# Optimization experiments

Measured on AMD Instinct MI355X. Metric: run time of the kernel, lower is better.

Reference implementation:

```python
import jax, jax.numpy as jnp
import numpy as np

NU, NI = 16384, 8192          # num_users, num_items
DK, DM = 64, 64               # embed_k, embed_k_multimod
DV, DT = 4096, 384            # visual / textual feature dims
TOP_K = 10
N_LAYERS = 1                  # item-graph propagation layers
N_UI_LAYERS = 2               # user-item LGConv layers
L_M = 0.7
E = 524288                    # user-item interactions (doubled to symmetric edges)


def build_sim(x):
    # cosine similarity: row-normalize then x @ x.T  -> [N, N]
    xn = x / jnp.linalg.norm(x, axis=-1, keepdims=True)
    return xn @ xn.T


def build_knn(sim, k):
    # keep top-k values per row, zero elsewhere (torch topk + scatter_)
    vals, idx = jax.lax.top_k(sim, k)
    rows = jnp.arange(sim.shape[0])[:, None]
    return jnp.zeros_like(sim).at[rows, idx].set(vals)


def normalized_laplacian(adj):
    # D^{-1/2} A D^{-1/2}; inf (zero-degree) -> 0, applied as row/col scaling
    d = adj.sum(-1)
    dis = jnp.where(d > 0, jax.lax.rsqrt(jnp.where(d > 0, d, 1.0)), 0.0)
    return adj * dis[:, None] * dis[None, :]


def l2_normalize(x, axis=-1, eps=1e-12):
    n = jnp.linalg.norm(x, axis=axis, keepdims=True)
    return x / jnp.maximum(n, eps)


def setup_inputs() -> dict:
    key = jax.random.key(0)
    ks = jax.random.split(key, 8)
    Gu = jax.random.normal(ks[0], (NU, DK), jnp.float32) * 0.1
    Gi = jax.random.normal(ks[1], (NI, DK), jnp.float32) * 0.1
    feat_v = jax.random.normal(ks[2], (NI, DV), jnp.float32)
    feat_t = jax.random.normal(ks[3], (NI, DT), jnp.float32)
    W_v = jax.random.normal(ks[4], (DV, DM), jnp.float32) / np.sqrt(DV)
    b_v = jnp.zeros((DM,), jnp.float32)
    W_t = jax.random.normal(ks[5], (DT, DM), jnp.float32) / np.sqrt(DT)
    b_t = jnp.zeros((DM,), jnp.float32)
    importance_weights = jnp.full((2,), 0.5, jnp.float32)
    # precomputed per-modality normalized laplacians from raw (detached) features
    Sim_v = normalized_laplacian(build_knn(build_sim(feat_v), TOP_K))
    Sim_t = normalized_laplacian(build_knn(build_sim(feat_t), TOP_K))
    # symmetric bipartite user-item edge list (items offset by NU)
    u = jax.random.randint(ks[6], (E,), 0, NU)
    i = jax.random.randint(ks[7], (E,), 0, NI) + NU
    edge_index = jnp.stack([jnp.concatenate([u, i]), jnp.concatenate([i, u])])
    return dict(Gu=Gu, Gi=Gi, feat_v=feat_v, feat_t=feat_t, W_v=W_v, b_v=b_v,
                W_t=W_t, b_t=b_t, importance_weights=importance_weights,
                Sim_v=Sim_v, Sim_t=Sim_t, edge_index=edge_index)


def propagate(Gu, Gi, feat_v, feat_t, W_v, b_v, W_t, b_t,
              importance_weights, Sim_v, Sim_t, edge_index):
    w = jax.nn.softmax(importance_weights)
    learned = jnp.zeros((NI, NI), jnp.float32)
    original = jnp.zeros((NI, NI), jnp.float32)
    for m, (feat, W, b, Sim) in enumerate(
            [(feat_v, W_v, b_v, Sim_v), (feat_t, W_t, b_t, Sim_t)]):
        proj = feat @ W + b                                  # [NI, DM]
        learned = learned + w[m] * build_knn(build_sim(proj), TOP_K)
        original = original + w[m] * Sim
    Si = (1.0 - L_M) * normalized_laplacian(learned) + L_M * original
    # item-graph propagation
    item_emb = Gi
    for _ in range(N_LAYERS):
        item_emb = Si @ item_emb                              # [NI, DK]
    # user-item LGConv (normalize=False => plain sum aggregation)
    src, dst = edge_index[0], edge_index[1]
    all_emb = [jnp.concatenate([Gu, Gi], 0)]                  # [NU+NI, DK]
    for _ in range(N_UI_LAYERS):
        agg = jax.ops.segment_sum(all_emb[-1][src], dst, num_segments=NU + NI)
        all_emb.append(l2_normalize(agg, axis=1))
    mean_emb = jnp.stack(all_emb, 1).mean(1)
    gu, gi = mean_emb[:NU], mean_emb[NU:]
    return gu, gi + l2_normalize(item_emb, axis=1)


def reference(Gu, Gi, feat_v, feat_t, W_v, b_v, W_t, b_t,
              importance_weights, Sim_v, Sim_t, edge_index):
    return propagate(Gu, Gi, feat_v, feat_t, W_v, b_v, W_t, b_t,
                     importance_weights, Sim_v, Sim_t, edge_index)
```

## Files before the change

### kernel.cpp

```cpp
#include <hip/hip_runtime.h>
#include <hip/hip_bf16.h>

#define NU 16384
#define NI 8192
#define TOPK 10
#define NTOT (NU + NI)
#define OCAP 64
#define NSEG 4
#define CSEG (NI / NSEG)
#define NGRP 512
#define MAXSEL 16

typedef short short8v __attribute__((ext_vector_type(8)));
typedef float float4v __attribute__((ext_vector_type(4)));

__device__ __forceinline__ float warp64_sum(float v) {
#pragma unroll
  for (int m = 32; m >= 1; m >>= 1) v += __shfl_xor(v, m);
  return v;
}

__device__ __forceinline__ unsigned int umap(float f) {
  unsigned int b = __float_as_uint(f);
  return b ^ ((b & 0x80000000u) ? 0xFFFFFFFFu : 0x80000000u);
}

__global__ __launch_bounds__(256) void proj_partial_kernel(
    const float* __restrict__ feat, const float* __restrict__ W,
    float* __restrict__ partial, int D, int kchunk) {
  __shared__ float sA[64][32];
  __shared__ float sB[64][68];
  const int tid = threadIdx.x;
  const int r0 = blockIdx.x * 32;
  const int ks = blockIdx.y;
  const int kb0v = ks * kchunk;
  const int rg = tid >> 4, cg = tid & 15;
  const int rA = tid & 31, kbA = (tid >> 5) * 8;
  const int kB = tid & 63, cbB = (tid >> 6) * 16;
  float acc[2][4] = {{0, 0, 0, 0}, {0, 0, 0, 0}};
  for (int kc = kb0v; kc < kb0v + kchunk; kc += 64) {
    const float* fp = feat + (size_t)(r0 + rA) * D + kc + kbA;
    float4 p0 = *(const float4*)fp;
    float4 p1 = *(const float4*)(fp + 4);
    sA[kbA + 0][rA] = p0.x; sA[kbA + 1][rA] = p0.y;
    sA[kbA + 2][rA] = p0.z; sA[kbA + 3][rA] = p0.w;
    sA[kbA + 4][rA] = p1.x; sA[kbA + 5][rA] = p1.y;
    sA[kbA + 6][rA] = p1.z; sA[kbA + 7][rA] = p1.w;
    const float* wp = W + (size_t)(kc + kB) * 64 + cbB;
    float4 q0 = *(const float4*)(wp + 0);
    float4 q1 = *(const float4*)(wp + 4);
    float4 q2 = *(const float4*)(wp + 8);
    float4 q3 = *(const float4*)(wp + 12);
    *(float4*)&sB[kB][cbB + 0] = q0;
    *(float4*)&sB[kB][cbB + 4] = q1;
    *(float4*)&sB[kB][cbB + 8] = q2;
    *(float4*)&sB[kB][cbB + 12] = q3;
    __syncthreads();
#pragma unroll 8
    for (int k = 0; k < 64; ++k) {
      float2 a = *(const float2*)&sA[k][rg * 2];
      float4 bv = *(const float4*)&sB[k][cg * 4];
      acc[0][0] += a.x * bv.x; acc[0][1] += a.x * bv.y;
      acc[0][2] += a.x * bv.z; acc[0][3] += a.x * bv.w;
      acc[1][0] += a.y * bv.x; acc[1][1] += a.y * bv.y;
      acc[1][2] += a.y * bv.z; acc[1][3] += a.y * bv.w;
    }
    __syncthreads();
  }
#pragma unroll
  for (int rr = 0; rr < 2; ++rr) {
    float4 o = make_float4(acc[rr][0], acc[rr][1], acc[rr][2], acc[rr][3]);
    *(float4*)(partial + ((size_t)ks * NI + r0 + rg * 2 + rr) * 64 + cg * 4) = o;
  }
}

__global__ __launch_bounds__(256) void proj_reduce_kernel(
    const float* __restrict__ partial, const float* __restrict__ b, int ksplit,
    float* __restrict__ xn, ushort* __restrict__ hi, ushort* __restrict__ lo) {
  const int row = blockIdx.x * 4 + (threadIdx.x >> 6);
  const int col = threadIdx.x & 63;
  float acc = b[col];
  for (int ks = 0; ks < ksplit; ++ks)
    acc += partial[((size_t)ks * NI + row) * 64 + col];
  float ss = warp64_sum(acc * acc);
  float v = acc * (1.0f / sqrtf(ss));
  xn[(size_t)row * 64 + col] = v;
  __hip_bfloat16 hb = __float2bfloat16(v);
  float hf = __bfloat162float(hb);
  __hip_bfloat16 lb = __float2bfloat16(v - hf);
  hi[(size_t)row * 64 + col] = *(ushort*)&hb;
  lo[(size_t)row * 64 + col] = *(ushort*)&lb;
}

__global__ __launch_bounds__(256) void sim_tilemax_kernel(
    const ushort* __restrict__ hiV, const ushort* __restrict__ loV,
    const ushort* __restrict__ hiT, const ushort* __restrict__ loT,
    float* __restrict__ tmax) {
  const int m = blockIdx.z;
  const ushort* hi = m ? hiT : hiV;
  const ushort* lo = m ? loT : loV;
  const int seg = blockIdx.y;
  const int c_base = seg * CSEG;
  const int r_base = blockIdx.x * 64;
  __shared__ ushort sH[64][64];
  __shared__ ushort sL[64][64];
  const int tid = threadIdx.x;
  const int wave = tid >> 6, lane = tid & 63;
  const int lr = lane & 15, lg = lane >> 4;
  const int my_row = r_base + wave * 16 + lr;
  short8v bh[2], bl[2];
  {
    const ushort* rp = hi + (size_t)my_row * 64 + lg * 8;
    bh[0] = *(const short8v*)(rp);
    bh[1] = *(const short8v*)(rp + 32);
    const ushort* rp2 = lo + (size_t)my_row * 64 + lg * 8;
    bl[0] = *(const short8v*)(rp2);
    bl[1] = *(const short8v*)(rp2 + 32);
  }
  float* tbase = tmax + ((size_t)m * NI + my_row) * NGRP + seg * (CSEG / 16);

  const int sc = tid >> 2, sq = (tid & 3) * 32;
  const int sw = (sc & 7) << 4;
  for (int c0 = 0; c0 < CSEG; c0 += 64) {
    __syncthreads();
    const char* gh = (const char*)(hi + (size_t)(c_base + c0 + sc) * 64);
    const char* gl2 = (const char*)(lo + (size_t)(c_base + c0 + sc) * 64);
    *(float4*)((char*)&sH[sc][0] + (sq ^ sw)) = *(const float4*)(gh + sq);
    *(float4*)((char*)&sH[sc][0] + ((sq + 16) ^ sw)) = *(const float4*)(gh + sq + 16);
    *(float4*)((char*)&sL[sc][0] + (sq ^ sw)) = *(const float4*)(gl2 + sq);
    *(float4*)((char*)&sL[sc][0] + ((sq + 16) ^ sw)) = *(const float4*)(gl2 + sq + 16);
    __syncthreads();
#pragma unroll
    for (int s = 0; s < 4; ++s) {
      const int ca = s * 16 + lr;
      const int cw = (ca & 7) << 4;
      const int kb0 = (lg * 16) ^ cw;
      const int kb1 = (lg * 16 + 64) ^ cw;
      short8v ah0 = *(const short8v*)((const char*)&sH[ca][0] + kb0);
      short8v ah1 = *(const short8v*)((const char*)&sH[ca][0] + kb1);
      short8v al0 = *(const short8v*)((const char*)&sL[ca][0] + kb0);
      short8v al1 = *(const short8v*)((const char*)&sL[ca][0] + kb1);
      float4v acc = {0.f, 0.f, 0.f, 0.f};
      acc = __builtin_amdgcn_mfma_f32_16x16x32_bf16(ah0, bh[0], acc, 0, 0, 0);
      acc = __builtin_amdgcn_mfma_f32_16x16x32_bf16(ah1, bh[1], acc, 0, 0, 0);
      acc = __builtin_amdgcn_mfma_f32_16x16x32_bf16(ah0, bl[0], acc, 0, 0, 0);
      acc = __builtin_amdgcn_mfma_f32_16x16x32_bf16(ah1, bl[1], acc, 0, 0, 0);
      acc = __builtin_amdgcn_mfma_f32_16x16x32_bf16(al0, bh[0], acc, 0, 0, 0);
      acc = __builtin_amdgcn_mfma_f32_16x16x32_bf16(al1, bh[1], acc, 0, 0, 0);
      float gm = fmaxf(fmaxf(acc[0], acc[1]), fmaxf(acc[2], acc[3]));
      gm = fmaxf(gm, __shfl_xor(gm, 16));
      gm = fmaxf(gm, __shfl_xor(gm, 32));
      if (lg == 0) tbase[(c0 >> 4) + s] = gm;
    }
  }
}

__global__ __launch_bounds__(256) void tile_rescore_kernel(
    const float* __restrict__ xn_v, const float* __restrict__ xn_t,
    const float* __restrict__ tmax,
    float* __restrict__ tkvV, int* __restrict__ tkiV,
    float* __restrict__ tkvT, int* __restrict__ tkiT) {
  const int bid = blockIdx.x;
  const int m = bid >> 13;
  const int row = bid & (NI - 1);
  const float* xn = m ? xn_t : xn_v;
  const int tid = threadIdx.x;
  __shared__ int ssel[MAXSEL];
  __shared__ float4 srq[16];
  __shared__ float sval[MAXSEL * 16];
  __shared__ int scol[MAXSEL * 16];
  __shared__ float lv[32];
  __shared__ int lc[32];
  __shared__ int lnum;
  if (tid < 64) {
    const int lane = tid;
    const float4* tmr4 = (const float4*)(tmax + ((size_t)m * NI + row) * NGRP);
    float4 t0 = tmr4[lane];
    float4 t1 = tmr4[64 + lane];
    unsigned int uv[8] = {umap(t0.x), umap(t0.y), umap(t0.z), umap(t0.w),
                          umap(t1.x), umap(t1.y), umap(t1.z), umap(t1.w)};
    unsigned long long blo = 0, bhi = 0x100000000ull;
    unsigned int taub = 0;
    for (int it = 0; it < 34; ++it) {
      unsigned int mid = (unsigned int)((blo + bhi) >> 1);
      int cnt = 0;
#pragma unroll
      for (int j = 0; j < 8; ++j) cnt += __popcll(__ballot(uv[j] >= mid));
      if (cnt >= 12) {
        taub = mid;
        if (cnt <= MAXSEL) break;
        blo = (unsigned long long)mid + 1;
      } else {
        bhi = mid;
      }
      if (blo >= bhi) break;
    }
    unsigned long long bj[8];
    int base[8];
    int tot = 0;
#pragma unroll
    for (int j = 0; j < 8; ++j) {
      bj[j] = __ballot(uv[j] >= taub);
      base[j] = tot;
      tot += __popcll(bj[j]);
    }
    if (lane < MAXSEL) ssel[lane] = -1;
    unsigned long long ltm = (1ull << lane) - 1ull;
#pragma unroll
    for (int j = 0; j < 8; ++j) {
      if (uv[j] >= taub) {
        int pos = base[j] + __popcll(bj[j] & ltm);
        if (pos < MAXSEL) {
          int g = (j < 4) ? (lane * 4 + j) : (256 + lane * 4 + (j - 4));
          ssel[pos] = g;
        }
      }
    }
  } else if (tid < 80) {
    srq[tid - 64] = ((const float4*)(xn + (size_t)row * 64))[tid - 64];
  }
  __syncthreads();
  {
    const int gsel = ssel[tid >> 4];
    const bool valid = (gsel >= 0);
    const int c = valid ? (gsel * 16 + (tid & 15)) : 0;
    const float4* cp = (const float4*)(xn + (size_t)c * 64);
    float acc = 0.0f;
#pragma unroll
    for (int k = 0; k < 16; ++k) {
      float4 a = srq[k];
      float4 bv = cp[k];
      acc += a.x * bv.x; acc += a.y * bv.y; acc += a.z * bv.z; acc += a.w * bv.w;
    }
    sval[tid] = valid ? acc : -3.0e38f;
    scol[tid] = valid ? c : 0x7fffffff;
  }
  __syncthreads();
  if (tid < 64) {
    const int lane = tid;
    float fv[4];
    int fc[4];
    unsigned int uv4[4];
#pragma unroll
    for (int k = 0; k < 4; ++k) {
      fv[k] = sval[lane + 64 * k];
      fc[k] = scol[lane + 64 * k];
      uv4[k] = umap(fv[k]);
    }
    unsigned long long blo = 0, bhi = 0x100000000ull;
    unsigned int taub = 0;
    for (int it = 0; it < 34; ++it) {
      unsigned int mid = (unsigned int)((blo + bhi) >> 1);
      int cnt = 0;
#pragma unroll
      for (int k = 0; k < 4; ++k) cnt += __popcll(__ballot(uv4[k] >= mid));
      if (cnt >= TOPK) {
        taub = mid;
        if (cnt == TOPK) break;
        blo = (unsigned long long)mid + 1;
      } else {
        bhi = mid;
      }
      if (blo >= bhi) break;
    }
    unsigned long long bk[4];
    int base[4];
    int tot = 0;
#pragma unroll
    for (int k = 0; k < 4; ++k) {
      bk[k] = __ballot(uv4[k] >= taub);
      base[k] = tot;
      tot += __popcll(bk[k]);
    }
    float* tv = m ? tkvT : tkvV;
    int* ti = m ? tkiT : tkiV;
    unsigned long long ltm = (1ull << lane) - 1ull;
    if (tot == TOPK) {
#pragma unroll
      for (int k = 0; k < 4; ++k) {
        if (uv4[k] >= taub) {
          int pos = base[k] + __popcll(bk[k] & ltm);
          tv[(size_t)row * TOPK + pos] = fv[k];
          ti[(size_t)row * TOPK + pos] = fc[k];
        }
      }
    } else {
#pragma unroll
      for (int k = 0; k < 4; ++k) {
        if (uv4[k] >= taub) {
          int pos = base[k] + __popcll(bk[k] & ltm);
          if (pos < 32) { lv[pos] = fv[k]; lc[pos] = fc[k]; }
        }
      }
      if (lane == 0) lnum = (tot < 32) ? tot : 32;
      if (lane == 0) {
        int n = lnum;
        unsigned int used = 0;
        for (int q = 0; q < TOPK; ++q) {
          float bv = -3.0e38f;
          int bc = 0x7fffffff, bi = -1;
          for (int i2 = 0; i2 < n; ++i2) {
            if (used & (1u << i2)) continue;
            if (lv[i2] > bv || (lv[i2] == bv && lc[i2] < bc)) {
              bv = lv[i2]; bc = lc[i2]; bi = i2;
            }
          }
          used |= (1u << bi);
          tv[(size_t)row * TOPK + q] = bv;
          ti[(size_t)row * TOPK + q] = bc;
        }
      }
    }
  }
}

__global__ void dis_kernel(const float* __restrict__ tkv_v, const float* __restrict__ tkv_t,
                           const float* __restrict__ iw, float* __restrict__ dis) {
  int r = blockIdx.x * blockDim.x + threadIdx.x;
  if (r >= NI) return;
  float ea = expf(iw[0]), eb = expf(iw[1]);
  float w0 = ea / (ea + eb), w1 = eb / (ea + eb);
  float s0 = 0.f, s1 = 0.f;
  for (int j = 0; j < TOPK; ++j) { s0 += tkv_v[r * TOPK + j]; s1 += tkv_t[r * TOPK + j]; }
  float d = w0 * s0 + w1 * s1;
  dis[r] = (d > 0.0f) ? (1.0f / sqrtf(d)) : 0.0f;
}

__global__ __launch_bounds__(256) void scan_sim_kernel(
    const float* __restrict__ Sv, const float* __restrict__ St,
    const float* __restrict__ iw, int* __restrict__ ocols,
    float* __restrict__ ow, int* __restrict__ ocnt) {
  const int lane = threadIdx.x & 63;
  const int row = blockIdx.x * 4 + (threadIdx.x >> 6);
  float ea = expf(iw[0]), eb = expf(iw[1]);
  float wA = 0.7f * ea / (ea + eb), wB = 0.7f * eb / (ea + eb);
  int cnt = 0;
  int* oc = ocols + (size_t)row * OCAP;
  float* op = ow + (size_t)row * OCAP;
#pragma unroll 1
  for (int m = 0; m < 2; ++m) {
    const float* S = m ? St : Sv;
    float wgt = m ? wB : wA;
    const float4* rp = (const float4*)(S + (size_t)row * NI);
    for (int it = 0; it < NI / 256; ++it) {
      float4 v = rp[it * 64 + lane];
      int cb = it * 256 + lane * 4;
#pragma unroll
      for (int j = 0; j < 4; ++j) {
        float x = (j == 0) ? v.x : (j == 1) ? v.y : (j == 2) ? v.z : v.w;
        bool nz = (x != 0.0f);
        unsigned long long mk = __ballot(nz);
        int pre = __popcll(mk & ((1ull << lane) - 1ull));
        if (nz) {
          int p = cnt + pre;
          if (p < OCAP) { oc[p] = cb + j; op[p] = wgt * x; }
        }
        cnt += __popcll(mk);
      }
    }
  }
  if (lane == 0) ocnt[row] = (cnt < OCAP) ? cnt : OCAP;
}

__global__ __launch_bounds__(256) void item_emb_kernel(
    const float* __restrict__ Gi,
    const float* __restrict__ tkv_v, const int* __restrict__ tki_v,
    const float* __restrict__ tkv_t, const int* __restrict__ tki_t,
    const float* __restrict__ dis, const int* __restrict__ ocols,
    const float* __restrict__ ow, const int* __restrict__ ocnt,
    const float* __restrict__ iw, float* __restrict__ nitem) {
  const int d = threadIdx.x & 63;
  const int row = blockIdx.x * 4 + (threadIdx.x >> 6);
  float ea = expf(iw[0]), eb = expf(iw[1]);
  float w0 = ea / (ea + eb), w1 = eb / (ea + eb);
  float disr = dis[row];
  float acc = 0.0f;
#pragma unroll 1
  for (int m = 0; m < 2; ++m) {
    const float* tv = m ? tkv_t : tkv_v;
    const int* ti = m ? tki_t : tki_v;
    float wm = (m ? w1 : w0) * 0.3f * disr;
    for (int j = 0; j < TOPK; ++j) {
      float val = tv[(size_t)row * TOPK + j];
      int c = ti[(size_t)row * TOPK + j];
      acc += wm * val * dis[c] * Gi[(size_t)c * 64 + d];
    }
  }
  int cn = ocnt[row];
  for (int j = 0; j < cn; ++j) {
    int c = ocols[(size_t)row * OCAP + j];
    float wv = ow[(size_t)row * OCAP + j];
    acc += wv * Gi[(size_t)c * 64 + d];
  }
  float ss = warp64_sum(acc * acc);
  float nr = sqrtf(ss);
  nitem[(size_t)row * 64 + d] = acc / fmaxf(nr, 1e-12f);
}

__global__ void hist_kernel(const int* __restrict__ dst, int* __restrict__ deg, int n) {
  int e = blockIdx.x * blockDim.x + threadIdx.x;
  if (e < n) atomicAdd(&deg[dst[e]], 1);
}

__global__ __launch_bounds__(256) void scanA_kernel(
    const int* __restrict__ deg, int* __restrict__ loc, int* __restrict__ bsum) {
  __shared__ int s[256];
  int tid = threadIdx.x, gid = blockIdx.x * 256 + tid;
  int x = deg[gid];
  s[tid] = x;
  __syncthreads();
  for (int off = 1; off < 256; off <<= 1) {
    int t = (tid >= off) ? s[tid - off] : 0;
    __syncthreads();
    s[tid] += t;
    __syncthreads();
  }
  loc[gid] = s[tid] - x;
  if (tid == 255) bsum[blockIdx.x] = s[255];
}

__global__ __launch_bounds__(256) void scanC_kernel(
    const int* __restrict__ loc, const int* __restrict__ bsum,
    int* __restrict__ row_ptr, int* __restrict__ cursor, int n) {
  int gid = blockIdx.x * blockDim.x + threadIdx.x;
  if (gid > n) return;
  int blk = gid >> 8;
  int off = 0;
  for (int b2 = 0; b2 < blk; ++b2) off += bsum[b2];
  if (gid == n) { row_ptr[n] = off; return; }
  int v = off + loc[gid];
  row_ptr[gid] = v;
  cursor[gid] = v;
}

__global__ void fill_kernel(const int* __restrict__ src, const int* __restrict__ dst,
                            int* __restrict__ cursor, int* __restrict__ csr, int n) {
  int e = blockIdx.x * blockDim.x + threadIdx.x;
  if (e < n) {
    int p = atomicAdd(&cursor[dst[e]], 1);
    csr[p] = src[e];
  }
}

__global__ __launch_bounds__(256) void segsum_kernel(
    const float* __restrict__ inU, const float* __restrict__ inI,
    const int* __restrict__ row_ptr, const int* __restrict__ csr,
    float* __restrict__ outp) {
  const int d = threadIdx.x & 63;
  const int row = blockIdx.x * 4 + (threadIdx.x >> 6);
  int a = row_ptr[row], bnd = row_ptr[row + 1];
  float acc = 0.0f;
  for (int e = a; e < bnd; ++e) {
    int s = csr[e];
    const float* sp = (s < NU) ? (inU + (size_t)s * 64) : (inI + (size_t)(s - NU) * 64);
    acc += sp[d];
  }
  float ss = warp64_sum(acc * acc);
  float nr = sqrtf(ss);
  outp[(size_t)row * 64 + d] = acc / fmaxf(nr, 1e-12f);
}

__global__ void final_kernel(const float* __restrict__ Gu, const float* __restrict__ Gi,
                             const float* __restrict__ e1b, const float* __restrict__ e2b,
                             const float* __restrict__ nitem, float* __restrict__ outp) {
  int idx = blockIdx.x * blockDim.x + threadIdx.x;
  int r = idx >> 6, d = idx & 63;
  float v0 = (r < NU) ? Gu[(size_t)r * 64 + d] : Gi[(size_t)(r - NU) * 64 + d];
  float v = (v0 + e1b[idx] + e2b[idx]) * (1.0f / 3.0f);
  if (r >= NU) v += nitem[(size_t)(r - NU) * 64 + d];
  outp[idx] = v;
}

extern "C" void kernel_launch(void* const* d_in, const int* in_sizes, int n_in,
                              void* d_out, int out_size, void* d_ws, size_t ws_size,
                              hipStream_t stream) {
  const float* Gu = (const float*)d_in[0];
  const float* Gi = (const float*)d_in[1];
  const float* feat_v = (const float*)d_in[2];
  const float* feat_t = (const float*)d_in[3];
  const float* W_v = (const float*)d_in[4];
  const float* b_v = (const float*)d_in[5];
  const float* W_t = (const float*)d_in[6];
  const float* b_t = (const float*)d_in[7];
  const float* iw = (const float*)d_in[8];
  const float* Sv = (const float*)d_in[9];
  const float* St = (const float*)d_in[10];
  const int* eidx = (const int*)d_in[11];
  const int twoE = in_sizes[11] / 2;
  const int* esrc = eidx;
  const int* edst = eidx + twoE;
  float* outp = (float*)d_out;

  char* w = (char*)d_ws;
  size_t off = 0;
  auto alloc = [&](size_t bytes) -> void* {
    void* p = w + off;
    off = (off + bytes + 255) & ~(size_t)255;
    return p;
  };
  float* xn_v = (float*)alloc((size_t)NI * 64 * 4);
  float* xn_t = (float*)alloc((size_t)NI * 64 * 4);
  ushort* hiV = (ushort*)alloc((size_t)NI * 64 * 2);
  ushort* loV = (ushort*)alloc((size_t)NI * 64 * 2);
  ushort* hiT = (ushort*)alloc((size_t)NI * 64 * 2);
  ushort* loT = (ushort*)alloc((size_t)NI * 64 * 2);
  float* tmax = (float*)alloc((size_t)2 * NI * NGRP * 4);
  float* tkvV = (float*)alloc((size_t)NI * TOPK * 4);
  int* tkiV = (int*)alloc((size_t)NI * TOPK * 4);
  float* tkvT = (float*)alloc((size_t)NI * TOPK * 4);
  int* tkiT = (int*)alloc((size_t)NI * TOPK * 4);
  float* dis = (float*)alloc((size_t)NI * 4);
  int* ocols = (int*)alloc((size_t)NI * OCAP * 4);
  float* ow = (float*)alloc((size_t)NI * OCAP * 4);
  int* ocnt = (int*)alloc((size_t)NI * 4);
  float* nitem = (float*)alloc((size_t)NI * 64 * 4);
  float* e1b = (float*)alloc((size_t)NTOT * 64 * 4);
  float* e2b = (float*)alloc((size_t)NTOT * 64 * 4);
  int* deg = (int*)alloc((size_t)NTOT * 4);
  int* row_ptr = (int*)alloc((size_t)(NTOT + 1) * 4);
  int* cursor = (int*)alloc((size_t)NTOT * 4);
  int* csr = (int*)alloc((size_t)twoE * 4);
  int* locb = (int*)alloc((size_t)NTOT * 4);
  int* bsum = (int*)alloc((size_t)(NTOT / 256) * 4);
  if (off > ws_size) return;

  float* partial = tmax;

  hipMemsetAsync(deg, 0, (size_t)NTOT * 4, stream);

  proj_partial_kernel<<<dim3(NI / 32, 8), 256, 0, stream>>>(feat_v, W_v, partial, 4096, 512);
  proj_reduce_kernel<<<NI / 4, 256, 0, stream>>>(partial, b_v, 8, xn_v, hiV, loV);
  proj_partial_kernel<<<dim3(NI / 32, 6), 256, 0, stream>>>(feat_t, W_t, partial, 384, 64);
  proj_reduce_kernel<<<NI / 4, 256, 0, stream>>>(partial, b_t, 6, xn_t, hiT, loT);
  sim_tilemax_kernel<<<dim3(NI / 64, NSEG, 2), 256, 0, stream>>>(hiV, loV, hiT, loT, tmax);
  tile_rescore_kernel<<<2 * NI, 256, 0, stream>>>(xn_v, xn_t, tmax, tkvV, tkiV,
                                                  tkvT, tkiT);
  dis_kernel<<<(NI + 255) / 256, 256, 0, stream>>>(tkvV, tkvT, iw, dis);
  scan_sim_kernel<<<NI / 4, 256, 0, stream>>>(Sv, St, iw, ocols, ow, ocnt);
  item_emb_kernel<<<NI / 4, 256, 0, stream>>>(Gi, tkvV, tkiV, tkvT, tkiT, dis, ocols, ow,
                                              ocnt, iw, nitem);
  hist_kernel<<<(twoE + 255) / 256, 256, 0, stream>>>(edst, deg, twoE);
  scanA_kernel<<<NTOT / 256, 256, 0, stream>>>(deg, locb, bsum);
  scanC_kernel<<<(NTOT + 1 + 255) / 256, 256, 0, stream>>>(locb, bsum, row_ptr, cursor, NTOT);
  fill_kernel<<<(twoE + 255) / 256, 256, 0, stream>>>(esrc, edst, cursor, csr, twoE);
  segsum_kernel<<<NTOT / 4, 256, 0, stream>>>(Gu, Gi, row_ptr, csr, e1b);
  segsum_kernel<<<NTOT / 4, 256, 0, stream>>>(e1b, e1b + (size_t)NU * 64, row_ptr, csr, e2b);
  final_kernel<<<(NTOT * 64) / 256, 256, 0, stream>>>(Gu, Gi, e1b, e2b, nitem, outp);
}
```

Before: 697.5 us.

## Enlarge projection GEMM tiles with prefetch, coalesce rescore loads, fuse final segsum

```diff
diff --git a/kernel.cpp b/kernel.cpp
--- a/kernel.cpp
+++ b/kernel.cpp
@@ -28,49 +28,58 @@
 __global__ __launch_bounds__(256) void proj_partial_kernel(
     const float* __restrict__ feat, const float* __restrict__ W,
     float* __restrict__ partial, int D, int kchunk) {
-  __shared__ float sA[64][32];
+  __shared__ float sA[64][64];
   __shared__ float sB[64][68];
   const int tid = threadIdx.x;
-  const int r0 = blockIdx.x * 32;
+  const int r0 = blockIdx.x * 64;
   const int ks = blockIdx.y;
-  const int kb0v = ks * kchunk;
   const int rg = tid >> 4, cg = tid & 15;
-  const int rA = tid & 31, kbA = (tid >> 5) * 8;
+  const int rA = tid & 63, kgA = (tid >> 6) * 16;
   const int kB = tid & 63, cbB = (tid >> 6) * 16;
-  float acc[2][4] = {{0, 0, 0, 0}, {0, 0, 0, 0}};
-  for (int kc = kb0v; kc < kb0v + kchunk; kc += 64) {
-    const float* fp = feat + (size_t)(r0 + rA) * D + kc + kbA;
-    float4 p0 = *(const float4*)fp;
-    float4 p1 = *(const float4*)(fp + 4);
-    sA[kbA + 0][rA] = p0.x; sA[kbA + 1][rA] = p0.y;
-    sA[kbA + 2][rA] = p0.z; sA[kbA + 3][rA] = p0.w;
-    sA[kbA + 4][rA] = p1.x; sA[kbA + 5][rA] = p1.y;
-    sA[kbA + 6][rA] = p1.z; sA[kbA + 7][rA] = p1.w;
-    const float* wp = W + (size_t)(kc + kB) * 64 + cbB;
-    float4 q0 = *(const float4*)(wp + 0);
-    float4 q1 = *(const float4*)(wp + 4);
-    float4 q2 = *(const float4*)(wp + 8);
-    float4 q3 = *(const float4*)(wp + 12);
-    *(float4*)&sB[kB][cbB + 0] = q0;
-    *(float4*)&sB[kB][cbB + 4] = q1;
-    *(float4*)&sB[kB][cbB + 8] = q2;
-    *(float4*)&sB[kB][cbB + 12] = q3;
+  const int kbeg = ks * kchunk, kend = kbeg + kchunk;
+  float4 pa[4], pb[4];
+  {
+    const float* fp = feat + (size_t)(r0 + rA) * D + kbeg + kgA;
+    pa[0] = *(const float4*)(fp + 0);  pa[1] = *(const float4*)(fp + 4);
+    pa[2] = *(const float4*)(fp + 8);  pa[3] = *(const float4*)(fp + 12);
+    const float* wp = W + (size_t)(kbeg + kB) * 64 + cbB;
+    pb[0] = *(const float4*)(wp + 0);  pb[1] = *(const float4*)(wp + 4);
+    pb[2] = *(const float4*)(wp + 8);  pb[3] = *(const float4*)(wp + 12);
+  }
+  float acc[4][4] = {{0,0,0,0},{0,0,0,0},{0,0,0,0},{0,0,0,0}};
+  for (int kc = kbeg; kc < kend; kc += 64) {
+#pragma unroll
+    for (int i = 0; i < 4; ++i) {
+      sA[kgA + 4*i + 0][rA] = pa[i].x;
+      sA[kgA + 4*i + 1][rA] = pa[i].y;
+      sA[kgA + 4*i + 2][rA] = pa[i].z;
+      sA[kgA + 4*i + 3][rA] = pa[i].w;
+      *(float4*)&sB[kB][cbB + 4*i] = pb[i];
+    }
     __syncthreads();
+    if (kc + 64 < kend) {
+      const float* fp = feat + (size_t)(r0 + rA) * D + kc + 64 + kgA;
+      pa[0] = *(const float4*)(fp + 0);  pa[1] = *(const float4*)(fp + 4);
+      pa[2] = *(const float4*)(fp + 8);  pa[3] = *(const float4*)(fp + 12);
+      const float* wp = W + (size_t)(kc + 64 + kB) * 64 + cbB;
+      pb[0] = *(const float4*)(wp + 0);  pb[1] = *(const float4*)(wp + 4);
+      pb[2] = *(const float4*)(wp + 8);  pb[3] = *(const float4*)(wp + 12);
+    }
 #pragma unroll 8
     for (int k = 0; k < 64; ++k) {
-      float2 a = *(const float2*)&sA[k][rg * 2];
-      float4 bv = *(const float4*)&sB[k][cg * 4];
-      acc[0][0] += a.x * bv.x; acc[0][1] += a.x * bv.y;
-      acc[0][2] += a.x * bv.z; acc[0][3] += a.x * bv.w;
-      acc[1][0] += a.y * bv.x; acc[1][1] += a.y * bv.y;
-      acc[1][2] += a.y * bv.z; acc[1][3] += a.y * bv.w;
+      float4 a = *(const float4*)&sA[k][rg * 4];
+      float4 b = *(const float4*)&sB[k][cg * 4];
+      acc[0][0] += a.x * b.x; acc[0][1] += a.x * b.y; acc[0][2] += a.x * b.z; acc[0][3] += a.x * b.w;
+      acc[1][0] += a.y * b.x; acc[1][1] += a.y * b.y; acc[1][2] += a.y * b.z; acc[1][3] += a.y * b.w;
+      acc[2][0] += a.z * b.x; acc[2][1] += a.z * b.y; acc[2][2] += a.z * b.z; acc[2][3] += a.z * b.w;
+      acc[3][0] += a.w * b.x; acc[3][1] += a.w * b.y; acc[3][2] += a.w * b.z; acc[3][3] += a.w * b.w;
     }
     __syncthreads();
   }
 #pragma unroll
-  for (int rr = 0; rr < 2; ++rr) {
+  for (int rr = 0; rr < 4; ++rr) {
     float4 o = make_float4(acc[rr][0], acc[rr][1], acc[rr][2], acc[rr][3]);
-    *(float4*)(partial + ((size_t)ks * NI + r0 + rg * 2 + rr) * 64 + cg * 4) = o;
+    *(float4*)(partial + ((size_t)ks * NI + r0 + rg * 4 + rr) * 64 + cg * 4) = o;
   }
 }
 
@@ -166,12 +175,13 @@
   const float* xn = m ? xn_t : xn_v;
   const int tid = threadIdx.x;
   __shared__ int ssel[MAXSEL];
-  __shared__ float4 srq[16];
   __shared__ float sval[MAXSEL * 16];
   __shared__ int scol[MAXSEL * 16];
   __shared__ float lv[32];
   __shared__ int lc[32];
   __shared__ int lnum;
+  const int grp = tid >> 4, l16 = tid & 15;
+  float4 rq = ((const float4*)(xn + (size_t)row * 64))[l16];
   if (tid < 64) {
     const int lane = tid;
     const float4* tmr4 = (const float4*)(tmax + ((size_t)m * NI + row) * NGRP);
@@ -216,24 +226,22 @@
         }
       }
     }
-  } else if (tid < 80) {
-    srq[tid - 64] = ((const float4*)(xn + (size_t)row * 64))[tid - 64];
   }
   __syncthreads();
-  {
-    const int gsel = ssel[tid >> 4];
-    const bool valid = (gsel >= 0);
-    const int c = valid ? (gsel * 16 + (tid & 15)) : 0;
-    const float4* cp = (const float4*)(xn + (size_t)c * 64);
-    float acc = 0.0f;
-#pragma unroll
-    for (int k = 0; k < 16; ++k) {
-      float4 a = srq[k];
-      float4 bv = cp[k];
-      acc += a.x * bv.x; acc += a.y * bv.y; acc += a.z * bv.z; acc += a.w * bv.w;
-    }
-    sval[tid] = valid ? acc : -3.0e38f;
-    scol[tid] = valid ? c : 0x7fffffff;
+  for (int it = 0; it < MAXSEL; ++it) {
+    int gsel = ssel[it];
+    bool valid = (gsel >= 0);
+    int c = valid ? (gsel * 16 + grp) : 0;
+    float4 x4 = ((const float4*)(xn + (size_t)c * 64))[l16];
+    float s = rq.x * x4.x + rq.y * x4.y + rq.z * x4.z + rq.w * x4.w;
+    s += __shfl_xor(s, 1);
+    s += __shfl_xor(s, 2);
+    s += __shfl_xor(s, 4);
+    s += __shfl_xor(s, 8);
+    if (l16 == 0) {
+      sval[it * 16 + grp] = valid ? s : -3.0e38f;
+      scol[it * 16 + grp] = valid ? c : 0x7fffffff;
+    }
   }
   __syncthreads();
   if (tid < 64) {
@@ -460,15 +468,28 @@
   outp[(size_t)row * 64 + d] = acc / fmaxf(nr, 1e-12f);
 }
 
-__global__ void final_kernel(const float* __restrict__ Gu, const float* __restrict__ Gi,
-                             const float* __restrict__ e1b, const float* __restrict__ e2b,
-                             const float* __restrict__ nitem, float* __restrict__ outp) {
-  int idx = blockIdx.x * blockDim.x + threadIdx.x;
-  int r = idx >> 6, d = idx & 63;
-  float v0 = (r < NU) ? Gu[(size_t)r * 64 + d] : Gi[(size_t)(r - NU) * 64 + d];
-  float v = (v0 + e1b[idx] + e2b[idx]) * (1.0f / 3.0f);
-  if (r >= NU) v += nitem[(size_t)(r - NU) * 64 + d];
-  outp[idx] = v;
+__global__ __launch_bounds__(256) void segsum_final_kernel(
+    const float* __restrict__ e1b, const int* __restrict__ row_ptr,
+    const int* __restrict__ csr, const float* __restrict__ Gu,
+    const float* __restrict__ Gi, const float* __restrict__ nitem,
+    float* __restrict__ outp) {
+  const int d = threadIdx.x & 63;
+  const int row = blockIdx.x * 4 + (threadIdx.x >> 6);
+  const float* inU = e1b;
+  const float* inI = e1b + (size_t)NU * 64;
+  int a = row_ptr[row], bnd = row_ptr[row + 1];
+  float acc = 0.0f;
+  for (int e = a; e < bnd; ++e) {
+    int s = csr[e];
+    const float* sp = (s < NU) ? (inU + (size_t)s * 64) : (inI + (size_t)(s - NU) * 64);
+    acc += sp[d];
+  }
+  float ss = warp64_sum(acc * acc);
+  float e2 = acc / fmaxf(sqrtf(ss), 1e-12f);
+  float base = (row < NU) ? Gu[(size_t)row * 64 + d] : Gi[(size_t)(row - NU) * 64 + d];
+  float v = (base + e1b[(size_t)row * 64 + d] + e2) * (1.0f / 3.0f);
+  if (row >= NU) v += nitem[(size_t)(row - NU) * 64 + d];
+  outp[(size_t)row * 64 + d] = v;
 }
 
 extern "C" void kernel_launch(void* const* d_in, const int* in_sizes, int n_in,
@@ -515,7 +536,6 @@
   int* ocnt = (int*)alloc((size_t)NI * 4);
   float* nitem = (float*)alloc((size_t)NI * 64 * 4);
   float* e1b = (float*)alloc((size_t)NTOT * 64 * 4);
-  float* e2b = (float*)alloc((size_t)NTOT * 64 * 4);
   int* deg = (int*)alloc((size_t)NTOT * 4);
   int* row_ptr = (int*)alloc((size_t)(NTOT + 1) * 4);
   int* cursor = (int*)alloc((size_t)NTOT * 4);
@@ -528,9 +548,9 @@
 
   hipMemsetAsync(deg, 0, (size_t)NTOT * 4, stream);
 
-  proj_partial_kernel<<<dim3(NI / 32, 8), 256, 0, stream>>>(feat_v, W_v, partial, 4096, 512);
+  proj_partial_kernel<<<dim3(NI / 64, 8), 256, 0, stream>>>(feat_v, W_v, partial, 4096, 512);
   proj_reduce_kernel<<<NI / 4, 256, 0, stream>>>(partial, b_v, 8, xn_v, hiV, loV);
-  proj_partial_kernel<<<dim3(NI / 32, 6), 256, 0, stream>>>(feat_t, W_t, partial, 384, 64);
+  proj_partial_kernel<<<dim3(NI / 64, 6), 256, 0, stream>>>(feat_t, W_t, partial, 384, 64);
   proj_reduce_kernel<<<NI / 4, 256, 0, stream>>>(partial, b_t, 6, xn_t, hiT, loT);
   sim_tilemax_kernel<<<dim3(NI / 64, NSEG, 2), 256, 0, stream>>>(hiV, loV, hiT, loT, tmax);
   tile_rescore_kernel<<<2 * NI, 256, 0, stream>>>(xn_v, xn_t, tmax, tkvV, tkiV,
@@ -544,6 +564,5 @@
   scanC_kernel<<<(NTOT + 1 + 255) / 256, 256, 0, stream>>>(locb, bsum, row_ptr, cursor, NTOT);
   fill_kernel<<<(twoE + 255) / 256, 256, 0, stream>>>(esrc, edst, cursor, csr, twoE);
   segsum_kernel<<<NTOT / 4, 256, 0, stream>>>(Gu, Gi, row_ptr, csr, e1b);
-  segsum_kernel<<<NTOT / 4, 256, 0, stream>>>(e1b, e1b + (size_t)NU * 64, row_ptr, csr, e2b);
-  final_kernel<<<(NTOT * 64) / 256, 256, 0, stream>>>(Gu, Gi, e1b, e2b, nitem, outp);
-}
+  segsum_final_kernel<<<NTOT / 4, 256, 0, stream>>>(e1b, row_ptr, csr, Gu, Gi, nitem, outp);
+}
```

Result: no change. 693.3 us (-0.6%).
